# Kernel tuning notes

Hardware: AMD Instinct MI355X
Metric: run time of the kernel (lower is better)

The kernel has to match this reference:

```python
import jax, jax.numpy as jnp
import numpy as np

T, D, F_, E, K = 8192, 1024, 4096, 8, 2


def setup_inputs() -> dict:
    key = jax.random.key(0)
    ks = jax.random.split(key, 5)
    s_d = 1.0 / np.sqrt(D)
    s_f = 1.0 / np.sqrt(F_)
    return {
        "x": jax.random.normal(ks[0], (T, D), dtype=jnp.float32),
        "gate_w": jax.random.normal(ks[1], (D, E), dtype=jnp.float32) * s_d,
        "w1": jax.random.normal(ks[2], (E, D, F_), dtype=jnp.float32) * s_d,  # up (gate proj)
        "w3": jax.random.normal(ks[3], (E, D, F_), dtype=jnp.float32) * s_d,  # up (value proj)
        "w2": jax.random.normal(ks[4], (E, F_, D), dtype=jnp.float32) * s_f,  # down proj
    }


def reference(x, gate_w, w1, w2, w3):
    # gate + top-k routing
    logits = x @ gate_w                                   # [T, E]
    top_w, top_idx = jax.lax.top_k(logits, K)             # [T, K]
    w = jax.nn.softmax(top_w.astype(jnp.float32), axis=-1).astype(x.dtype)
    # combine[t, e] = routing weight of token t for expert e (0 if unrouted)
    combine = jnp.sum(w[:, :, None] * jax.nn.one_hot(top_idx, E, dtype=x.dtype), axis=1)  # [T, E]
    # dense dispatch: each expert processes all tokens, masked by combine weight
    # (identical math to the torch gather/scatter loop: unrouted tokens get weight 0)
    out = jnp.zeros_like(x)
    for e in range(E):
        h = jax.nn.silu(x @ w1[e]) * (x @ w3[e])          # [T, F] SwiGLU
        out = out + combine[:, e:e + 1] * (h @ w2[e])     # [T, D]
    return out
```

## Files before the change

kernel.cpp:

```cpp
#include <hip/hip_runtime.h>
#include <stdint.h>

#define T_TOK 8192
#define D_DIM 1024
#define F_DIM 4096
#define E_NUM 8
#define RCAP  17408
#define MT    136

typedef __bf16 bf16;
typedef __bf16 bf16x8 __attribute__((ext_vector_type(8)));
typedef float  f32x4  __attribute__((ext_vector_type(4)));

typedef const __attribute__((address_space(1))) void* gptr1;
typedef __attribute__((address_space(3))) void* lptr3;

__device__ __forceinline__ void gload_lds16(const void* g, void* l) {
    __builtin_amdgcn_global_load_lds((gptr1)g, (lptr3)l, 16, 0, 0);
}

__device__ __forceinline__ unsigned short f2b(float f) {
    uint32_t u = __float_as_uint(f);
    u = (u + 0x7FFFu + ((u >> 16) & 1u)) >> 16;
    return (unsigned short)u;
}

__global__ __launch_bounds__(256) void trans_kernel(const float* __restrict__ src,
                                                    bf16* __restrict__ dst,
                                                    int R, int C) {
    __shared__ unsigned short lt[64 * 72];
    const int e  = blockIdx.z;
    const int c0 = blockIdx.x * 64;
    const int r0 = blockIdx.y * 64;
    const float* s = src + (size_t)e * R * C;
    unsigned short* dp = (unsigned short*)dst + (size_t)e * R * C;
    const int t  = threadIdx.x;
    const int tr = t >> 4;
    const int tc = (t & 15) * 4;
    #pragma unroll
    for (int rr = 0; rr < 4; ++rr) {
        const int r = tr + rr * 16;
        const float4 v = *(const float4*)(s + (size_t)(r0 + r) * C + c0 + tc);
        lt[(tc + 0) * 72 + r] = f2b(v.x);
        lt[(tc + 1) * 72 + r] = f2b(v.y);
        lt[(tc + 2) * 72 + r] = f2b(v.z);
        lt[(tc + 3) * 72 + r] = f2b(v.w);
    }
    __syncthreads();
    const int oc  = t >> 2;
    const int seg = (t & 3) * 16;
    const uint4 a = *(const uint4*)&lt[oc * 72 + seg];
    const uint4 b = *(const uint4*)&lt[oc * 72 + seg + 8];
    unsigned short* orow = dp + (size_t)(c0 + oc) * R + (r0 + seg);
    *(uint4*)(orow)     = a;
    *(uint4*)(orow + 8) = b;
}

__global__ __launch_bounds__(256) void gate_kernel(const float* __restrict__ x,
                                                   const float* __restrict__ gw,
                                                   int* __restrict__ tki,
                                                   float* __restrict__ tkw,
                                                   int* __restrict__ counts) {
    const int t    = blockIdx.x * 4 + (threadIdx.x >> 6);
    const int lane = threadIdx.x & 63;
    const float* xr = x + (size_t)t * D_DIM;
    float acc[E_NUM];
    #pragma unroll
    for (int e = 0; e < E_NUM; ++e) acc[e] = 0.f;
    for (int j = 0; j < 16; ++j) {
        const int d = lane + 64 * j;
        const float xv = xr[d];
        const float* g = gw + (size_t)d * E_NUM;
        #pragma unroll
        for (int e = 0; e < E_NUM; ++e) acc[e] += xv * g[e];
    }
    #pragma unroll
    for (int off = 32; off >= 1; off >>= 1) {
        #pragma unroll
        for (int e = 0; e < E_NUM; ++e) acc[e] += __shfl_xor(acc[e], off);
    }
    if (lane == 0) {
        int b0 = 0; float v0 = acc[0];
        #pragma unroll
        for (int e = 1; e < E_NUM; ++e) if (acc[e] > v0) { v0 = acc[e]; b0 = e; }
        int b1 = -1; float v1 = -1e30f;
        #pragma unroll
        for (int e = 0; e < E_NUM; ++e) if (e != b0 && acc[e] > v1) { v1 = acc[e]; b1 = e; }
        const float ex = expf(v1 - v0);
        const float w0 = 1.f / (1.f + ex);
        const float w1 = ex * w0;
        tki[t * 2]     = b0;  tkw[t * 2]     = w0;
        tki[t * 2 + 1] = b1;  tkw[t * 2 + 1] = w1;
        atomicAdd(&counts[b0], 1);
        atomicAdd(&counts[b1], 1);
    }
}

__global__ void scan_kernel(const int* __restrict__ counts, int* __restrict__ aoff,
                            int* __restrict__ cursor) {
    if (threadIdx.x == 0) {
        int off = 0;
        #pragma unroll
        for (int e = 0; e < E_NUM; ++e) {
            aoff[e]   = off;
            cursor[e] = off;
            off += (counts[e] + 127) & ~127;
        }
        aoff[E_NUM] = off;
    }
}

__global__ __launch_bounds__(256) void gather_kernel(const float* __restrict__ x,
                                                     const int* __restrict__ tki,
                                                     int* __restrict__ cursor,
                                                     int* __restrict__ s2r,
                                                     bf16* __restrict__ xp) {
    const int slot = blockIdx.x * 4 + (threadIdx.x >> 6);
    const int lane = threadIdx.x & 63;
    const int t = slot >> 1;
    int row = 0;
    if (lane == 0) {
        const int e = tki[slot];
        row = atomicAdd(&cursor[e], 1);
        s2r[slot] = row;
    }
    row = __shfl(row, 0);
    const float* xr = x + (size_t)t * D_DIM + lane * 16;
    unsigned short* dst = (unsigned short*)xp + (size_t)row * D_DIM + lane * 16;
    uint32_t u[8];
    #pragma unroll
    for (int q = 0; q < 4; ++q) {
        const float4 v = *(const float4*)(xr + q * 4);
        u[q * 2]     = (uint32_t)f2b(v.x) | ((uint32_t)f2b(v.y) << 16);
        u[q * 2 + 1] = (uint32_t)f2b(v.z) | ((uint32_t)f2b(v.w) << 16);
    }
    ((uint4*)dst)[0] = make_uint4(u[0], u[1], u[2], u[3]);
    ((uint4*)dst)[1] = make_uint4(u[4], u[5], u[6], u[7]);
}

__global__ __launch_bounds__(256, 2) void gemm1_kernel(const bf16* __restrict__ xp,
                                                       const bf16* __restrict__ wb1t,
                                                       const bf16* __restrict__ wb3t,
                                                       bf16* __restrict__ hb,
                                                       const int* __restrict__ aoff,
                                                       const int* __restrict__ counts) {
    __shared__ bf16 As[128 * 32];
    __shared__ bf16 Bs1[128 * 32];
    __shared__ bf16 Bs3[128 * 32];

    const int m_base = blockIdx.y * 128;
    int e = 0;
    #pragma unroll
    for (int i = 1; i < E_NUM; ++i) if (m_base >= aoff[i]) e = i;
    if (m_base - aoff[e] >= counts[e]) return;

    const int nt   = blockIdx.x;
    const int tid  = threadIdx.x;
    const int w    = tid >> 6;
    const int lane = tid & 63;
    const int wm   = w & 1, wn = w >> 1;

    const bf16* Ab = xp + (size_t)m_base * D_DIM;
    const bf16* B1 = wb1t + ((size_t)e * F_DIM + (size_t)nt * 128) * D_DIM;
    const bf16* B3 = wb3t + ((size_t)e * F_DIM + (size_t)nt * 128) * D_DIM;

    const int lr16 = lane >> 2;
    const int cg   = lane & 3;
    const int srow = w * 32 + lr16;
    const int scol = (cg ^ ((lr16 >> 1) & 3)) * 8;
    const int ldsbase = w * 1024;
    const int fm = lane & 15;
    const int fk = (((lane >> 4) ^ ((fm >> 1) & 3))) * 8;

    f32x4 acc1[4][4] = {};
    f32x4 acc3[4][4] = {};

    for (int kt = 0; kt < D_DIM / 32; ++kt) {
        const int k0 = kt * 32;
        #pragma unroll
        for (int j = 0; j < 2; ++j) {
            const size_t go = (size_t)(srow + j * 16) * D_DIM + (k0 + scol);
            gload_lds16(Ab + go, &As[ldsbase + j * 512]);
            gload_lds16(B1 + go, &Bs1[ldsbase + j * 512]);
            gload_lds16(B3 + go, &Bs3[ldsbase + j * 512]);
        }
        __syncthreads();
        bf16x8 af[4], b1f[4], b3f[4];
        #pragma unroll
        for (int i = 0; i < 4; ++i) {
            af[i]  = *(const bf16x8*)&As [(wm * 64 + i * 16 + fm) * 32 + fk];
            b1f[i] = *(const bf16x8*)&Bs1[(wn * 64 + i * 16 + fm) * 32 + fk];
            b3f[i] = *(const bf16x8*)&Bs3[(wn * 64 + i * 16 + fm) * 32 + fk];
        }
        #pragma unroll
        for (int i = 0; i < 4; ++i) {
            #pragma unroll
            for (int jn = 0; jn < 4; ++jn) {
                acc1[i][jn] = __builtin_amdgcn_mfma_f32_16x16x32_bf16(af[i], b1f[jn], acc1[i][jn], 0, 0, 0);
                acc3[i][jn] = __builtin_amdgcn_mfma_f32_16x16x32_bf16(af[i], b3f[jn], acc3[i][jn], 0, 0, 0);
            }
        }
        __syncthreads();
    }

    unsigned short* hw = (unsigned short*)hb;
    #pragma unroll
    for (int i = 0; i < 4; ++i) {
        const int rbase = m_base + wm * 64 + i * 16 + (lane >> 4) * 4;
        #pragma unroll
        for (int jn = 0; jn < 4; ++jn) {
            const int col = nt * 128 + wn * 64 + jn * 16 + (lane & 15);
            #pragma unroll
            for (int r = 0; r < 4; ++r) {
                const float s1 = acc1[i][jn][r];
                const float s3 = acc3[i][jn][r];
                const float hv = (s1 / (1.0f + __expf(-s1))) * s3;
                hw[(size_t)(rbase + r) * F_DIM + col] = f2b(hv);
            }
        }
    }
}

__global__ __launch_bounds__(256, 2) void gemm2_kernel(const bf16* __restrict__ hb,
                                                       const bf16* __restrict__ wb2t,
                                                       float* __restrict__ yb,
                                                       const int* __restrict__ aoff,
                                                       const int* __restrict__ counts) {
    __shared__ bf16 As[128 * 32];
    __shared__ bf16 Bs[128 * 32];

    const int m_base = blockIdx.y * 128;
    int e = 0;
    #pragma unroll
    for (int i = 1; i < E_NUM; ++i) if (m_base >= aoff[i]) e = i;
    if (m_base - aoff[e] >= counts[e]) return;

    const int nt   = blockIdx.x;
    const int tid  = threadIdx.x;
    const int w    = tid >> 6;
    const int lane = tid & 63;
    const int wm   = w & 1, wn = w >> 1;

    const bf16* Ab = hb + (size_t)m_base * F_DIM;
    const bf16* Bb = wb2t + ((size_t)e * D_DIM + (size_t)nt * 128) * F_DIM;

    const int lr16 = lane >> 2;
    const int cg   = lane & 3;
    const int srow = w * 32 + lr16;
    const int scol = (cg ^ ((lr16 >> 1) & 3)) * 8;
    const int ldsbase = w * 1024;
    const int fm = lane & 15;
    const int fk = (((lane >> 4) ^ ((fm >> 1) & 3))) * 8;

    f32x4 acc[4][4] = {};

    for (int kt = 0; kt < F_DIM / 32; ++kt) {
        const int k0 = kt * 32;
        #pragma unroll
        for (int j = 0; j < 2; ++j) {
            const size_t go = (size_t)(srow + j * 16) * F_DIM + (k0 + scol);
            gload_lds16(Ab + go, &As[ldsbase + j * 512]);
            gload_lds16(Bb + go, &Bs[ldsbase + j * 512]);
        }
        __syncthreads();
        bf16x8 af[4], bfr[4];
        #pragma unroll
        for (int i = 0; i < 4; ++i) {
            af[i]  = *(const bf16x8*)&As[(wm * 64 + i * 16 + fm) * 32 + fk];
            bfr[i] = *(const bf16x8*)&Bs[(wn * 64 + i * 16 + fm) * 32 + fk];
        }
        #pragma unroll
        for (int i = 0; i < 4; ++i) {
            #pragma unroll
            for (int jn = 0; jn < 4; ++jn) {
                acc[i][jn] = __builtin_amdgcn_mfma_f32_16x16x32_bf16(af[i], bfr[jn], acc[i][jn], 0, 0, 0);
            }
        }
        __syncthreads();
    }

    #pragma unroll
    for (int i = 0; i < 4; ++i) {
        const int rb = m_base + wm * 64 + i * 16 + (lane >> 4) * 4;
        #pragma unroll
        for (int r = 0; r < 4; ++r) {
            float* yrow = yb + (size_t)(rb + r) * D_DIM;
            #pragma unroll
            for (int jn = 0; jn < 4; ++jn) {
                const int col = nt * 128 + wn * 64 + jn * 16 + (lane & 15);
                yrow[col] = acc[i][jn][r];
            }
        }
    }
}

__global__ __launch_bounds__(256) void combine_kernel(const float* __restrict__ yb,
                                                      const int* __restrict__ s2r,
                                                      const float* __restrict__ tkw,
                                                      float* __restrict__ out) {
    const int idx = blockIdx.x * 256 + threadIdx.x;
    const int t = idx >> 8;
    const int c = (idx & 255) * 4;
    const int r0 = s2r[t * 2], r1 = s2r[t * 2 + 1];
    const float w0 = tkw[t * 2], w1 = tkw[t * 2 + 1];
    const float4 a = *(const float4*)(yb + (size_t)r0 * D_DIM + c);
    const float4 b = *(const float4*)(yb + (size_t)r1 * D_DIM + c);
    float4 o;
    o.x = w0 * a.x + w1 * b.x;
    o.y = w0 * a.y + w1 * b.y;
    o.z = w0 * a.z + w1 * b.z;
    o.w = w0 * a.w + w1 * b.w;
    *(float4*)(out + (size_t)t * D_DIM + c) = o;
}

extern "C" void kernel_launch(void* const* d_in, const int* in_sizes, int n_in,
                              void* d_out, int out_size, void* d_ws, size_t ws_size,
                              hipStream_t stream) {
    const float* x  = (const float*)d_in[0];
    const float* gw = (const float*)d_in[1];
    const float* w1 = (const float*)d_in[2];
    const float* w3 = (const float*)d_in[3];
    const float* w2 = (const float*)d_in[4];
    float* out = (float*)d_out;

    char* ws = (char*)d_ws;
    size_t off = 0;
    bf16* wb1t = (bf16*)(ws + off);
    bf16* wb2t = wb1t;
    off += (size_t)E_NUM * F_DIM * D_DIM * 2;
    bf16* wb3t = (bf16*)(ws + off);
    float* yb  = (float*)wb3t;
    off += (size_t)E_NUM * F_DIM * D_DIM * 2;
    bf16* xp   = (bf16*)(ws + off); off += (size_t)RCAP * D_DIM * 2;
    bf16* hb   = (bf16*)(ws + off); off += (size_t)RCAP * F_DIM * 2;
    int*   tki = (int*)(ws + off);   off += (size_t)T_TOK * 2 * 4;
    float* tkw = (float*)(ws + off); off += (size_t)T_TOK * 2 * 4;
    int* counts = (int*)(ws + off);  off += 64;
    int* cursor = (int*)(ws + off);  off += 64;
    int* aoff   = (int*)(ws + off);  off += 64;
    int* s2r    = (int*)(ws + off);  off += (size_t)T_TOK * 2 * 4;

    hipMemsetAsync(counts, 0, 64, stream);

    gate_kernel<<<T_TOK / 4, 256, 0, stream>>>(x, gw, tki, tkw, counts);
    scan_kernel<<<1, 64, 0, stream>>>(counts, aoff, cursor);
    gather_kernel<<<(T_TOK * 2) / 4, 256, 0, stream>>>(x, tki, cursor, s2r, xp);

    trans_kernel<<<dim3(F_DIM / 64, D_DIM / 64, E_NUM), 256, 0, stream>>>(w1, wb1t, D_DIM, F_DIM);
    trans_kernel<<<dim3(F_DIM / 64, D_DIM / 64, E_NUM), 256, 0, stream>>>(w3, wb3t, D_DIM, F_DIM);

    gemm1_kernel<<<dim3(F_DIM / 128, MT), 256, 0, stream>>>(xp, wb1t, wb3t, hb, aoff, counts);

    trans_kernel<<<dim3(D_DIM / 64, F_DIM / 64, E_NUM), 256, 0, stream>>>(w2, wb2t, F_DIM, D_DIM);

    gemm2_kernel<<<dim3(D_DIM / 128, MT), 256, 0, stream>>>(hb, wb2t, yb, aoff, counts);

    combine_kernel<<<(T_TOK * 256) / 256, 256, 0, stream>>>(yb, s2r, tkw, out);
}
```

Before: 1.402 ms.

## Rewrite gemm1 with 256x256 tiles, interleaved w1/w3 weights, and double-buffered LDS

The transpose kernel now writes w1 and w3 into one buffer, interleaved in 32-row groups, so gemm1 streams a single B operand. gemm1 moves to 512 threads with 256x256 output tiles and 64-wide K steps, double-buffered in LDS via global_load_lds. It splits MFMA work into quarter phases with barriers, s_setprio and explicit waitcnts so loads overlap compute, and assigns m-blocks per expert to drop empty tiles. The goal is more data reuse per byte loaded and hidden memory latency. The cost is 128KB of LDS per block, which limits occupancy to one block per CU, plus fragile hand-written wait counts and masking of tail rows.

Measured after the change: 1.412 ms. No clear change (+0.8%).

```diff
diff --git a/kernel.cpp b/kernel.cpp
--- a/kernel.cpp
+++ b/kernel.cpp
@@ -27,13 +27,13 @@
 
 __global__ __launch_bounds__(256) void trans_kernel(const float* __restrict__ src,
                                                     bf16* __restrict__ dst,
-                                                    int R, int C) {
+                                                    int R, int C, int mode) {
     __shared__ unsigned short lt[64 * 72];
     const int e  = blockIdx.z;
     const int c0 = blockIdx.x * 64;
     const int r0 = blockIdx.y * 64;
     const float* s = src + (size_t)e * R * C;
-    unsigned short* dp = (unsigned short*)dst + (size_t)e * R * C;
+    unsigned short* dp = (unsigned short*)dst + (size_t)e * R * C * (mode ? 2 : 1);
     const int t  = threadIdx.x;
     const int tr = t >> 4;
     const int tc = (t & 15) * 4;
@@ -51,7 +51,9 @@
     const int seg = (t & 3) * 16;
     const uint4 a = *(const uint4*)&lt[oc * 72 + seg];
     const uint4 b = *(const uint4*)&lt[oc * 72 + seg + 8];
-    unsigned short* orow = dp + (size_t)(c0 + oc) * R + (r0 + seg);
+    const int f  = c0 + oc;
+    const int fr = mode ? ((f >> 5) * 64 + ((mode == 2) ? 32 : 0) + (f & 31)) : f;
+    unsigned short* orow = dp + (size_t)fr * R + (r0 + seg);
     *(uint4*)(orow)     = a;
     *(uint4*)(orow + 8) = b;
 }
@@ -138,87 +140,184 @@
     ((uint4*)dst)[1] = make_uint4(u[4], u[5], u[6], u[7]);
 }
 
-__global__ __launch_bounds__(256, 2) void gemm1_kernel(const bf16* __restrict__ xp,
-                                                       const bf16* __restrict__ wb1t,
-                                                       const bf16* __restrict__ wb3t,
+__global__ __launch_bounds__(512, 2) void gemm1_kernel(const bf16* __restrict__ xp,
+                                                       const bf16* __restrict__ wb13t,
                                                        bf16* __restrict__ hb,
                                                        const int* __restrict__ aoff,
                                                        const int* __restrict__ counts) {
-    __shared__ bf16 As[128 * 32];
-    __shared__ bf16 Bs1[128 * 32];
-    __shared__ bf16 Bs3[128 * 32];
-
-    const int m_base = blockIdx.y * 128;
-    int e = 0;
-    #pragma unroll
-    for (int i = 1; i < E_NUM; ++i) if (m_base >= aoff[i]) e = i;
-    if (m_base - aoff[e] >= counts[e]) return;
-
-    const int nt   = blockIdx.x;
+    __shared__ __align__(16) char As[65536];
+    __shared__ __align__(16) char Bs[65536];
+
+    const int nt = blockIdx.x;
+    int bm = blockIdx.y;
+    int e  = 0;
+    for (; e < E_NUM; ++e) {
+        const int nbi = (counts[e] + 255) >> 8;
+        if (bm < nbi) break;
+        bm -= nbi;
+    }
+    if (e >= E_NUM) return;
+    const int m_base = aoff[e] + bm * 256;
+    const int row_hi = aoff[e + 1];
+
     const int tid  = threadIdx.x;
     const int w    = tid >> 6;
     const int lane = tid & 63;
-    const int wm   = w & 1, wn = w >> 1;
-
-    const bf16* Ab = xp + (size_t)m_base * D_DIM;
-    const bf16* B1 = wb1t + ((size_t)e * F_DIM + (size_t)nt * 128) * D_DIM;
-    const bf16* B3 = wb3t + ((size_t)e * F_DIM + (size_t)nt * 128) * D_DIM;
-
-    const int lr16 = lane >> 2;
-    const int cg   = lane & 3;
-    const int srow = w * 32 + lr16;
-    const int scol = (cg ^ ((lr16 >> 1) & 3)) * 8;
-    const int ldsbase = w * 1024;
-    const int fm = lane & 15;
-    const int fk = (((lane >> 4) ^ ((fm >> 1) & 3))) * 8;
-
-    f32x4 acc1[4][4] = {};
-    f32x4 acc3[4][4] = {};
-
-    for (int kt = 0; kt < D_DIM / 32; ++kt) {
-        const int k0 = kt * 32;
+    const int wm   = w >> 2;
+    const int wn   = w & 3;
+
+    const int    lsub = lane >> 3;
+    const size_t swz  = (size_t)(((lane & 7) ^ lsub) << 3);
+    const bf16* Ag = xp    + (size_t)m_base * D_DIM;
+    const bf16* Bg = wb13t + ((size_t)e * (2 * F_DIM) + (size_t)nt * 256) * D_DIM;
+    char* sAd = As + w * 2048 + lane * 16;
+    char* sBd = Bs + w * 2048 + lane * 16;
+    const int rst = w * 16 + lsub;
+
+#define G1_STAGE_A(cc, kt, h)                                                         \
+    do {                                                                              \
+        const size_t kcol = (size_t)(kt) * 64 + swz;                                  \
+        gload_lds16(Ag + (size_t)((h) * 128 + rst) * D_DIM + kcol,                    \
+                    sAd + (cc) * 32768 + (h) * 16384);                                \
+        gload_lds16(Ag + (size_t)((h) * 128 + rst + 8) * D_DIM + kcol,                \
+                    sAd + (cc) * 32768 + (h) * 16384 + 1024);                         \
+    } while (0)
+#define G1_STAGE_B(cc, kt, h)                                                         \
+    do {                                                                              \
+        const size_t kcol = (size_t)(kt) * 64 + swz;                                  \
+        gload_lds16(Bg + (size_t)((h) * 128 + rst) * D_DIM + kcol,                    \
+                    sBd + (cc) * 32768 + (h) * 16384);                                \
+        gload_lds16(Bg + (size_t)((h) * 128 + rst + 8) * D_DIM + kcol,                \
+                    sBd + (cc) * 32768 + (h) * 16384 + 1024);                         \
+    } while (0)
+
+    const int fm  = lane & 15;
+    const int kq  = lane >> 4;
+    const int kg0 = ((kq       ^ (fm & 7)) << 4);
+    const int kg1 = (((4 | kq) ^ (fm & 7)) << 4);
+    const char* Arb = As + wm * 16384 + fm * 128;
+    const char* Brb = Bs + (wn >> 1) * 16384 + ((wn & 1) * 64 + fm) * 128;
+
+    f32x4 acc[8][4] = {};
+    bf16x8 aF[4][2], b0F[2][2], b1F[2][2];
+
+    G1_STAGE_A(0, 0, 0); G1_STAGE_A(0, 0, 1);
+    G1_STAGE_B(0, 0, 0); G1_STAGE_B(0, 0, 1);
+    G1_STAGE_B(1, 1, 0); G1_STAGE_B(1, 1, 1);
+    asm volatile("s_waitcnt vmcnt(4)" ::: "memory");
+    __builtin_amdgcn_s_barrier();
+    __builtin_amdgcn_sched_barrier(0);
+
+    for (int u = 0; u < D_DIM / 64; ++u) {
+        const int c = u & 1;
+        const char* Ar = Arb + c * 32768;
+        const char* Br = Brb + c * 32768;
+
+        #pragma unroll
+        for (int i = 0; i < 4; ++i) {
+            aF[i][0] = *(const bf16x8*)(Ar + i * 2048 + kg0);
+            aF[i][1] = *(const bf16x8*)(Ar + i * 2048 + kg1);
+        }
         #pragma unroll
         for (int j = 0; j < 2; ++j) {
-            const size_t go = (size_t)(srow + j * 16) * D_DIM + (k0 + scol);
-            gload_lds16(Ab + go, &As[ldsbase + j * 512]);
-            gload_lds16(B1 + go, &Bs1[ldsbase + j * 512]);
-            gload_lds16(B3 + go, &Bs3[ldsbase + j * 512]);
-        }
-        __syncthreads();
-        bf16x8 af[4], b1f[4], b3f[4];
+            b0F[j][0] = *(const bf16x8*)(Br + j * 2048 + kg0);
+            b0F[j][1] = *(const bf16x8*)(Br + j * 2048 + kg1);
+        }
+        if (u + 1 < D_DIM / 64) G1_STAGE_A(c ^ 1, u + 1, 0);
+        __builtin_amdgcn_s_barrier();
+        asm volatile("s_waitcnt lgkmcnt(0)" ::: "memory");
+        __builtin_amdgcn_s_setprio(1);
+        #pragma unroll
+        for (int i = 0; i < 4; ++i)
+            #pragma unroll
+            for (int j = 0; j < 2; ++j) {
+                acc[i][j] = __builtin_amdgcn_mfma_f32_16x16x32_bf16(aF[i][0], b0F[j][0], acc[i][j], 0, 0, 0);
+                acc[i][j] = __builtin_amdgcn_mfma_f32_16x16x32_bf16(aF[i][1], b0F[j][1], acc[i][j], 0, 0, 0);
+            }
+        __builtin_amdgcn_s_setprio(0);
+        __builtin_amdgcn_s_barrier();
+
+        #pragma unroll
+        for (int j = 0; j < 2; ++j) {
+            b1F[j][0] = *(const bf16x8*)(Br + (j + 2) * 2048 + kg0);
+            b1F[j][1] = *(const bf16x8*)(Br + (j + 2) * 2048 + kg1);
+        }
+        if (u + 1 < D_DIM / 64) G1_STAGE_A(c ^ 1, u + 1, 1);
+        __builtin_amdgcn_s_barrier();
+        asm volatile("s_waitcnt lgkmcnt(0)" ::: "memory");
+        __builtin_amdgcn_s_setprio(1);
+        #pragma unroll
+        for (int i = 0; i < 4; ++i)
+            #pragma unroll
+            for (int j = 0; j < 2; ++j) {
+                acc[i][j + 2] = __builtin_amdgcn_mfma_f32_16x16x32_bf16(aF[i][0], b1F[j][0], acc[i][j + 2], 0, 0, 0);
+                acc[i][j + 2] = __builtin_amdgcn_mfma_f32_16x16x32_bf16(aF[i][1], b1F[j][1], acc[i][j + 2], 0, 0, 0);
+            }
+        __builtin_amdgcn_s_setprio(0);
+        __builtin_amdgcn_s_barrier();
+
         #pragma unroll
         for (int i = 0; i < 4; ++i) {
-            af[i]  = *(const bf16x8*)&As [(wm * 64 + i * 16 + fm) * 32 + fk];
-            b1f[i] = *(const bf16x8*)&Bs1[(wn * 64 + i * 16 + fm) * 32 + fk];
-            b3f[i] = *(const bf16x8*)&Bs3[(wn * 64 + i * 16 + fm) * 32 + fk];
-        }
-        #pragma unroll
-        for (int i = 0; i < 4; ++i) {
-            #pragma unroll
-            for (int jn = 0; jn < 4; ++jn) {
-                acc1[i][jn] = __builtin_amdgcn_mfma_f32_16x16x32_bf16(af[i], b1f[jn], acc1[i][jn], 0, 0, 0);
-                acc3[i][jn] = __builtin_amdgcn_mfma_f32_16x16x32_bf16(af[i], b3f[jn], acc3[i][jn], 0, 0, 0);
-            }
-        }
-        __syncthreads();
+            aF[i][0] = *(const bf16x8*)(Ar + (i + 4) * 2048 + kg0);
+            aF[i][1] = *(const bf16x8*)(Ar + (i + 4) * 2048 + kg1);
+        }
+        if (u + 2 < D_DIM / 64) G1_STAGE_B(c, u + 2, 0);
+        __builtin_amdgcn_s_barrier();
+        asm volatile("s_waitcnt lgkmcnt(0)" ::: "memory");
+        __builtin_amdgcn_s_setprio(1);
+        #pragma unroll
+        for (int i = 0; i < 4; ++i)
+            #pragma unroll
+            for (int j = 0; j < 2; ++j) {
+                acc[i + 4][j] = __builtin_amdgcn_mfma_f32_16x16x32_bf16(aF[i][0], b0F[j][0], acc[i + 4][j], 0, 0, 0);
+                acc[i + 4][j] = __builtin_amdgcn_mfma_f32_16x16x32_bf16(aF[i][1], b0F[j][1], acc[i + 4][j], 0, 0, 0);
+            }
+        __builtin_amdgcn_s_setprio(0);
+        __builtin_amdgcn_s_barrier();
+
+        if (u + 2 < D_DIM / 64) G1_STAGE_B(c, u + 2, 1);
+        __builtin_amdgcn_s_setprio(1);
+        #pragma unroll
+        for (int i = 0; i < 4; ++i)
+            #pragma unroll
+            for (int j = 0; j < 2; ++j) {
+                acc[i + 4][j + 2] = __builtin_amdgcn_mfma_f32_16x16x32_bf16(aF[i][0], b1F[j][0], acc[i + 4][j + 2], 0, 0, 0);
+                acc[i + 4][j + 2] = __builtin_amdgcn_mfma_f32_16x16x32_bf16(aF[i][1], b1F[j][1], acc[i + 4][j + 2], 0, 0, 0);
+            }
+        __builtin_amdgcn_s_setprio(0);
+
+        if (u == D_DIM / 64 - 1) break;
+        if (u + 2 < D_DIM / 64) {
+            asm volatile("s_waitcnt vmcnt(4)" ::: "memory");
+        } else {
+            asm volatile("s_waitcnt vmcnt(0)" ::: "memory");
+        }
+        __builtin_amdgcn_s_barrier();
+        __builtin_amdgcn_sched_barrier(0);
     }
 
     unsigned short* hw = (unsigned short*)hb;
-    #pragma unroll
-    for (int i = 0; i < 4; ++i) {
-        const int rbase = m_base + wm * 64 + i * 16 + (lane >> 4) * 4;
-        #pragma unroll
-        for (int jn = 0; jn < 4; ++jn) {
-            const int col = nt * 128 + wn * 64 + jn * 16 + (lane & 15);
-            #pragma unroll
-            for (int r = 0; r < 4; ++r) {
-                const float s1 = acc1[i][jn][r];
-                const float s3 = acc3[i][jn][r];
-                const float hv = (s1 / (1.0f + __expf(-s1))) * s3;
-                hw[(size_t)(rbase + r) * F_DIM + col] = f2b(hv);
-            }
-        }
-    }
+    const int g    = nt * 4 + wn;
+    const int colb = g * 32 + fm;
+    const int rb0  = m_base + wm * 128 + (kq << 2);
+    #pragma unroll
+    for (int i = 0; i < 8; ++i) {
+        #pragma unroll
+        for (int r = 0; r < 4; ++r) {
+            const int row = rb0 + i * 16 + r;
+            if (row < row_hi) {
+                #pragma unroll
+                for (int jj = 0; jj < 2; ++jj) {
+                    const float s1 = acc[i][jj][r];
+                    const float s3 = acc[i][jj + 2][r];
+                    const float hv = (s1 / (1.0f + __expf(-s1))) * s3;
+                    hw[(size_t)row * F_DIM + colb + jj * 16] = f2b(hv);
+                }
+            }
+        }
+    }
+#undef G1_STAGE_A
+#undef G1_STAGE_B
 }
 
 __global__ __launch_bounds__(256, 2) void gemm2_kernel(const bf16* __restrict__ hb,
@@ -324,15 +423,12 @@
     float* out = (float*)d_out;
 
     char* ws = (char*)d_ws;
-    size_t off = 0;
-    bf16* wb1t = (bf16*)(ws + off);
-    bf16* wb2t = wb1t;
-    off += (size_t)E_NUM * F_DIM * D_DIM * 2;
-    bf16* wb3t = (bf16*)(ws + off);
-    float* yb  = (float*)wb3t;
-    off += (size_t)E_NUM * F_DIM * D_DIM * 2;
-    bf16* xp   = (bf16*)(ws + off); off += (size_t)RCAP * D_DIM * 2;
-    bf16* hb   = (bf16*)(ws + off); off += (size_t)RCAP * F_DIM * 2;
+    bf16*  wb13t = (bf16*)(ws);
+    bf16*  wb2t  = (bf16*)(ws);
+    float* yb    = (float*)(ws + (size_t)67108864);
+    bf16*  xp    = (bf16*)(ws + (size_t)134217728);
+    size_t off   = (size_t)134217728 + (size_t)RCAP * D_DIM * 2;
+    bf16*  hb    = (bf16*)(ws + off); off += (size_t)RCAP * F_DIM * 2;
     int*   tki = (int*)(ws + off);   off += (size_t)T_TOK * 2 * 4;
     float* tkw = (float*)(ws + off); off += (size_t)T_TOK * 2 * 4;
     int* counts = (int*)(ws + off);  off += 64;
@@ -346,12 +442,12 @@
     scan_kernel<<<1, 64, 0, stream>>>(counts, aoff, cursor);
     gather_kernel<<<(T_TOK * 2) / 4, 256, 0, stream>>>(x, tki, cursor, s2r, xp);
 
-    trans_kernel<<<dim3(F_DIM / 64, D_DIM / 64, E_NUM), 256, 0, stream>>>(w1, wb1t, D_DIM, F_DIM);
-    trans_kernel<<<dim3(F_DIM / 64, D_DIM / 64, E_NUM), 256, 0, stream>>>(w3, wb3t, D_DIM, F_DIM);
-
-    gemm1_kernel<<<dim3(F_DIM / 128, MT), 256, 0, stream>>>(xp, wb1t, wb3t, hb, aoff, counts);
-
-    trans_kernel<<<dim3(D_DIM / 64, F_DIM / 64, E_NUM), 256, 0, stream>>>(w2, wb2t, F_DIM, D_DIM);
+    trans_kernel<<<dim3(F_DIM / 64, D_DIM / 64, E_NUM), 256, 0, stream>>>(w1, wb13t, D_DIM, F_DIM, 1);
+    trans_kernel<<<dim3(F_DIM / 64, D_DIM / 64, E_NUM), 256, 0, stream>>>(w3, wb13t, D_DIM, F_DIM, 2);
+
+    gemm1_kernel<<<dim3(2 * F_DIM / 256, 72), 512, 0, stream>>>(xp, wb13t, hb, aoff, counts);
+
+    trans_kernel<<<dim3(D_DIM / 64, F_DIM / 64, E_NUM), 256, 0, stream>>>(w2, wb2t, F_DIM, D_DIM, 0);
 
     gemm2_kernel<<<dim3(D_DIM / 128, MT), 256, 0, stream>>>(hb, wb2t, yb, aoff, counts);
 
```
